# Kernel tuning notes

Measured on AMD Instinct MI355X. Metric: run time of the kernel, lower is better.

Reference implementation:

```python
import jax, jax.numpy as jnp
import numpy as np
import math

B, N, D = 64, 128, 128          # graphs, nodes per graph, d_model
D_STATE = 2                     # Mamba default d_state
D_CONV = 4                      # Mamba default conv kernel
DT_RANK = math.ceil(D / 16)     # 8
CUTOFF = 10.0
N_GAUSS = 50                    # GaussianSmearing(0, 10, 50)
EPS_RMS = 1e-5


def setup_inputs() -> dict:
    key = jax.random.key(0)
    ks = jax.random.split(key, 12)
    s = 0.05
    inp = {}
    inp['x'] = jax.random.normal(ks[0], (B * N, D), jnp.float32)
    inp['pos'] = jax.random.normal(ks[1], (B * N, 3), jnp.float32) * 5.0
    inp['map_idx'] = jax.random.randint(ks[2], (B * N,), 0, 16)
    inp['batch'] = jnp.repeat(jnp.arange(B), N)
    # RMSNorm
    inp['norm_w'] = jnp.ones((D,), jnp.float32)
    # simple message-passing gnn (stand-in for injected gnn module)
    inp['gnn_w1'] = jax.random.normal(ks[3], (D, D), jnp.float32) * s
    inp['gnn_b1'] = jnp.zeros((D,), jnp.float32)
    inp['gnn_w2'] = jax.random.normal(ks[4], (D, D), jnp.float32) * s
    inp['gnn_b2'] = jnp.zeros((D,), jnp.float32)
    # Linear(50, 1) on Gaussian-smeared edge distances
    inp['lin_w'] = jax.random.normal(ks[5], (N_GAUSS, 1), jnp.float32) * s
    inp['lin_b'] = jnp.zeros((1,), jnp.float32)
    # MambaBlock params (stored [in, out])
    inp['in_proj_w'] = jax.random.normal(ks[6], (D, 2 * D), jnp.float32) * s
    inp['conv_w'] = jax.random.normal(ks[7], (D, D_CONV), jnp.float32) * s
    inp['conv_b'] = jnp.zeros((D,), jnp.float32)
    inp['x_proj_w'] = jax.random.normal(ks[8], (D, DT_RANK + 2 * D_STATE), jnp.float32) * s
    inp['dt_proj_w'] = jax.random.normal(ks[9], (DT_RANK, D), jnp.float32) * s
    inp['dt_proj_b'] = jnp.zeros((D,), jnp.float32)
    inp['A_log'] = jnp.log(jnp.tile(jnp.arange(1, D_STATE + 1, dtype=jnp.float32), (D, 1)))
    inp['D_param'] = jnp.ones((D,), jnp.float32)
    inp['out_proj_w'] = jax.random.normal(ks[10], (D, D), jnp.float32) * s
    return inp


def _rmsnorm(x, w):
    return x * jax.lax.rsqrt(jnp.mean(x * x, axis=-1, keepdims=True) + EPS_RMS) * w


def _mamba(x_t, adj, in_proj_w, conv_w, conv_b, x_proj_w, dt_proj_w, dt_proj_b,
           A_log, D_param, out_proj_w):
    # x_t: [N, D] node sequence for one graph; adj: [N, N] dense edge-value matrix
    L = x_t.shape[0]
    A = -jnp.exp(A_log)                                   # [D, S]
    xr = x_t @ in_proj_w                                  # [L, 2D]
    xm, res = xr[:, :D], xr[:, D:]
    # causal depthwise conv1d (padding d_conv-1, truncated to L)
    xp = jnp.pad(xm, ((D_CONV - 1, 0), (0, 0)))
    xc = conv_b + sum(xp[j:j + L] * conv_w[:, j] for j in range(D_CONV))
    xc = jax.nn.silu(xc)                                  # [L, D]
    dbl = xc @ x_proj_w                                   # [L, dt_rank + 2S]
    delta = dbl[:, :DT_RANK]
    Bm = dbl[:, DT_RANK:DT_RANK + D_STATE]                # [L, S]
    Cm = dbl[:, DT_RANK + D_STATE:]                       # [L, S]
    delta = jax.nn.softplus(delta @ dt_proj_w + dt_proj_b)  # [L, D]
    # temp_adj_padded: ones [D, D] with adjacency slice in top-left
    m = min(L, D)
    adj_pad = jnp.ones((D, D), dtype=adj.dtype).at[:m, :m].set(adj[:m, :m])
    delta_p = delta @ adj_pad                             # [L, D]
    dA = jnp.exp(delta_p[:, :, None] * A[None])           # [L, D, S]
    dBu = delta_p[:, :, None] * Bm[:, None, :] * xc[:, :, None]

    def step(h, t):
        dA_t, dBu_t, C_t = t
        h = dA_t * h + dBu_t                              # [D, S]
        return h, h @ C_t                                 # [D]

    _, ys = jax.lax.scan(step, jnp.zeros((D, D_STATE), x_t.dtype), (dA, dBu, Cm))
    y = ys + xc * D_param
    y = y * jax.nn.silu(res)
    out = y @ out_proj_w
    return jnp.where(jnp.isfinite(out), out, 0.0)


def reference(x, pos, map_idx, batch, norm_w, gnn_w1, gnn_b1, gnn_w2, gnn_b2,
              lin_w, lin_b, in_proj_w, conv_w, conv_b, x_proj_w, dt_proj_w,
              dt_proj_b, A_log, D_param, out_proj_w):
    x1 = _rmsnorm(x, norm_w)                              # [B*N, D]
    xg = x1.reshape(B, N, D)
    pg = pos.reshape(B, N, 3)
    # per-graph radius graph (dense): dist + edge mask
    diff = pg[:, :, None, :] - pg[:, None, :, :]          # [B, N, N, 3]
    d2 = jnp.sum(diff * diff, axis=-1)
    eye = jnp.eye(N, dtype=bool)[None]
    dist = jnp.sqrt(jnp.where(eye, 1.0, d2))              # safe sqrt on diag
    edge_mask = (~eye) & (dist < CUTOFF)                  # [B, N, N]
    em = edge_mask.astype(x1.dtype)
    # simple message-passing gnn: mean-aggregate relu(Wx) over radius neighbors
    h = jax.nn.relu(xg @ gnn_w1 + gnn_b1)
    deg = jnp.clip(jnp.sum(em, axis=-1, keepdims=True), 1.0, None)
    agg = jnp.einsum('bij,bjd->bid', em, h) / deg
    x2 = agg @ gnn_w2 + gnn_b2                            # [B, N, D]
    # GaussianSmearing(0, 10, 50) + Linear(50, 1) -> dense edge-value matrix
    offsets = jnp.linspace(0.0, 10.0, N_GAUSS)
    coeff = -0.5 / (offsets[1] - offsets[0]) ** 2
    smear = jnp.exp(coeff * (dist[..., None] - offsets) ** 2)  # [B, N, N, 50]
    d_dense = smear @ lin_w[:, 0] + lin_b[0]
    adj = jnp.where(edge_mask, d_dense, 0.0)              # sparse-to-dense
    # Mamba mixer over each graph's node sequence
    mix = jax.vmap(lambda xt, a: _mamba(xt, a, in_proj_w, conv_w, conv_b,
                                        x_proj_w, dt_proj_w, dt_proj_b,
                                        A_log, D_param, out_proj_w))
    x3 = mix(x2, adj).reshape(B * N, D)
    output = x3 + x1
    return (output, pos, map_idx)
```

## Files before the change

### kernel.cpp

```cpp
#include <hip/hip_runtime.h>
#include <math.h>

#define B_ 64
#define N_ 128
#define D_ 128
#define BN_ 8192
#define NG_ 50
#define CUTOFF_ 10.0f

typedef __attribute__((ext_vector_type(8))) short short8v;
typedef __attribute__((ext_vector_type(4))) float f32x4;
#define MFMA16 __builtin_amdgcn_mfma_f32_16x16x32_bf16

__device__ __forceinline__ float bf2f(unsigned short h) {
    return __builtin_bit_cast(float, ((unsigned int)h) << 16);
}
__device__ __forceinline__ unsigned short f2bf(float f) {
    unsigned int u = __builtin_bit_cast(unsigned int, f);
    return (unsigned short)((u + 0x7FFFu + ((u >> 16) & 1u)) >> 16);
}
__device__ __forceinline__ void splitbf(float x, unsigned short& h, unsigned short& l) {
    h = f2bf(x);
    l = f2bf(x - bf2f(h));
}
__device__ __forceinline__ void gl_lds(const void* g, void* l) {
    __builtin_amdgcn_global_load_lds(
        (const __attribute__((address_space(1))) void*)g,
        (__attribute__((address_space(3))) void*)l, 16, 0, 0);
}

__global__ __launch_bounds__(256) void setup_k(
        const float* __restrict__ x, const float* __restrict__ norm_w,
        const float* __restrict__ pos, const int* __restrict__ mi,
        const float* __restrict__ lin_w, const float* __restrict__ lin_b,
        const float* __restrict__ w1, const float* __restrict__ w2,
        const float* __restrict__ b2, const float* __restrict__ in_proj,
        const float* __restrict__ xpw, const float* __restrict__ dtw,
        const float* __restrict__ out_proj,
        unsigned short* __restrict__ w1Th, unsigned short* __restrict__ w1Tl,
        unsigned short* __restrict__ WdTh, unsigned short* __restrict__ WdTl,
        unsigned short* __restrict__ opTh, unsigned short* __restrict__ opTl,
        unsigned short* __restrict__ WfTh, unsigned short* __restrict__ WfTl,
        float* __restrict__ bfv,
        float* __restrict__ x1f, unsigned short* __restrict__ x1h,
        unsigned short* __restrict__ x1l,
        unsigned short* __restrict__ adjh, unsigned short* __restrict__ adjl,
        unsigned short* __restrict__ emh, float* __restrict__ rdeg,
        float* __restrict__ out) {
    int blk = blockIdx.x, t = threadIdx.x;
    if (blk < 513) {
        if (blk < 128) {
            if (t < 128) {
                unsigned short h, l;
                splitbf(w1[blk * 128 + t], h, l);
                w1Th[t * 128 + blk] = h; w1Tl[t * 128 + blk] = l;
            }
        } else if (blk < 256) {
            int m = blk - 128;
            if (t < 128) {
                float s = 0.0f;
                #pragma unroll
                for (int r = 0; r < 8; r++) s = fmaf(xpw[m * 12 + r], dtw[r * 128 + t], s);
                unsigned short h, l; splitbf(s, h, l);
                WdTh[t * 128 + m] = h; WdTl[t * 128 + m] = l;
            }
        } else if (blk < 384) {
            int k = blk - 256;
            if (t < 128) {
                unsigned short h, l;
                splitbf(out_proj[k * 128 + t], h, l);
                opTh[t * 128 + k] = h; opTl[t * 128 + k] = l;
            }
        } else if (blk < 512) {
            int k = blk - 384;
            float s = 0.0f;
            #pragma unroll 8
            for (int j = 0; j < 128; j++) s = fmaf(w2[k * 128 + j], in_proj[j * 256 + t], s);
            unsigned short h, l; splitbf(s, h, l);
            WfTh[t * 128 + k] = h; WfTl[t * 128 + k] = l;
        } else {
            float s = 0.0f;
            #pragma unroll 8
            for (int j = 0; j < 128; j++) s = fmaf(b2[j], in_proj[j * 256 + t], s);
            bfv[t] = s;
        }
    } else if (blk < 642) {
        int idx = (blk - 513) * 256 + t;
        if (idx < BN_ * 3) out[(size_t)BN_ * D_ + idx] = pos[idx];
        if (idx < BN_) out[(size_t)BN_ * D_ + BN_ * 3 + idx] = (float)mi[idx];
    } else if (blk < 2690) {
        int rblk = blk - 642;
        int wv = t >> 6, ln = t & 63;
        int row = rblk * 4 + wv;
        const float2* xr = reinterpret_cast<const float2*>(x) + (size_t)row * 64;
        float2 v = xr[ln];
        float s = fmaf(v.x, v.x, v.y * v.y);
        #pragma unroll
        for (int o = 32; o > 0; o >>= 1) s += __shfl_down(s, o, 64);
        float tot = __shfl(s, 0, 64);
        float r = rsqrtf(tot * (1.0f / D_) + 1e-5f);
        float2 wv2 = reinterpret_cast<const float2*>(norm_w)[ln];
        float o0 = v.x * r * wv2.x, o1 = v.y * r * wv2.y;
        reinterpret_cast<float2*>(x1f)[(size_t)row * 64 + ln] = make_float2(o0, o1);
        unsigned short h0, l0, h1, l1;
        splitbf(o0, h0, l0); splitbf(o1, h1, l1);
        reinterpret_cast<ushort2*>(x1h)[(size_t)row * 64 + ln] = make_ushort2(h0, h1);
        reinterpret_cast<ushort2*>(x1l)[(size_t)row * 64 + ln] = make_ushort2(l0, l1);
    } else {
        __shared__ float px[N_], py[N_], pz[N_];
        __shared__ float lw[NG_];
        __shared__ int degs[8];
        int ablk = blk - 2690;
        int bx = ablk & 15, b = ablk >> 4;
        if (t < N_) {
            const float* p = pos + (size_t)(b * N_ + t) * 3;
            px[t] = p[0]; py[t] = p[1]; pz[t] = p[2];
        } else if (t - N_ < NG_) {
            lw[t - N_] = lin_w[t - N_];
        }
        if (t >= 248) degs[t - 248] = 0;
        __syncthreads();
        float linb = lin_b[0];
        int j = t & 127;
        int il = t >> 7;
        const float DEL = 10.0f / 49.0f;
        const float COEFF = -0.5f / (DEL * DEL);
        #pragma unroll
        for (int p = 0; p < 4; p++) {
            int i = bx * 8 + p * 2 + il;
            float dx = px[i] - px[j], dy = py[i] - py[j], dz = pz[i] - pz[j];
            float d2 = dx * dx + dy * dy + dz * dz;
            float dist = (i == j) ? 1.0f : sqrtf(d2);
            bool edge = (i != j) && (dist < CUTOFF_);
            float val = 0.0f;
            if (edge) {
                int g0 = (int)ceilf((dist - 1.75f) / DEL); if (g0 < 0) g0 = 0;
                int g1 = (int)floorf((dist + 1.75f) / DEL); if (g1 > NG_ - 1) g1 = NG_ - 1;
                float dm = dist - (float)g0 * DEL;
                float tg = expf(COEFF * dm * dm);
                float ug = expf(COEFF * DEL * (DEL - 2.0f * dm));
                float s = linb;
                for (int g = g0; g <= g1; g++) {
                    s = fmaf(lw[g], tg, s);
                    tg *= ug;
                    ug *= 0.36787944117144233f;
                }
                val = s;
            }
            size_t idx = ((size_t)b * N_ + i) * N_ + j;
            unsigned short h, l; splitbf(val, h, l);
            adjh[idx] = h; adjl[idx] = l;
            emh[idx] = edge ? 0x3F80 : 0;
            unsigned long long msk = __ballot(edge);
            if ((t & 63) == 0) atomicAdd(&degs[p * 2 + il], __popcll(msk));
        }
        __syncthreads();
        if (t < 8) {
            int dg = degs[t];
            rdeg[(size_t)b * N_ + bx * 8 + t] = 1.0f / (float)(dg > 0 ? dg : 1);
        }
    }
}

#define AHOFF 0
#define ALOFF 8192
#define BHOFF 16384
#define BLOFF 32768
template <int EPI, bool ALO>
__global__ __launch_bounds__(256, 3) void mgemm_k(
        const unsigned short* __restrict__ Ah, const unsigned short* __restrict__ Al,
        const unsigned short* __restrict__ BTh, const unsigned short* __restrict__ BTl,
        const float* __restrict__ bias, const float* __restrict__ AUX,
        float* __restrict__ Cf, unsigned short* __restrict__ Ch,
        unsigned short* __restrict__ Cl, int cstride, int wbs) {
    extern __shared__ char sm[];
    int tid = threadIdx.x;
    int row_base = blockIdx.x * 32;
    int col_base = blockIdx.y * 64;

    const unsigned short* pBh = BTh;
    const unsigned short* pBl = BTl;
    if (wbs) {
        size_t bo = (size_t)(row_base >> 7) * (size_t)wbs;
        pBh += bo; pBl += bo;
    }

    #pragma unroll
    for (int i = 0; i < 2; i++) {
        int s = tid + i * 256;
        int row = s >> 4, inner = s & 15;
        int gb = (inner * 16) ^ ((row & 7) << 4);
        size_t gsrc = (size_t)(row_base + row) * 256 + gb;
        gl_lds((const char*)Ah + gsrc, sm + AHOFF + s * 16);
        if (ALO) gl_lds((const char*)Al + gsrc, sm + ALOFF + s * 16);
    }
    #pragma unroll
    for (int i = 0; i < 4; i++) {
        int s = tid + i * 256;
        int n = s >> 4, inner = s & 15;
        int gb = (inner * 16) ^ ((n & 7) << 4);
        size_t gsrc = (size_t)(col_base + n) * 256 + gb;
        gl_lds((const char*)pBh + gsrc, sm + BHOFF + s * 16);
        gl_lds((const char*)pBl + gsrc, sm + BLOFF + s * 16);
    }
    __syncthreads();

    int w = tid >> 6, l = tid & 63;
    int rlow = l & 15, kb_lane = (l >> 4) * 16;
    int nB = w * 16 + rlow;
    int nswz = (nB & 7) << 4;
    f32x4 acc[2] = {{0.f, 0.f, 0.f, 0.f}, {0.f, 0.f, 0.f, 0.f}};
    #pragma unroll
    for (int kb = 0; kb < 4; kb++) {
        int kbyte = kb * 64 + kb_lane;
        short8v bh = *(const short8v*)(sm + BHOFF + nB * 256 + (kbyte ^ nswz));
        short8v bl = *(const short8v*)(sm + BLOFF + nB * 256 + (kbyte ^ nswz));
        #pragma unroll
        for (int rf = 0; rf < 2; rf++) {
            int ra = rf * 16 + rlow;
            int aswz = (ra & 7) << 4;
            short8v ah = *(const short8v*)(sm + AHOFF + ra * 256 + (kbyte ^ aswz));
            acc[rf] = MFMA16(ah, bh, acc[rf], 0, 0, 0);
            acc[rf] = MFMA16(ah, bl, acc[rf], 0, 0, 0);
            if (ALO) {
                short8v al_ = *(const short8v*)(sm + ALOFF + ra * 256 + (kbyte ^ aswz));
                acc[rf] = MFMA16(al_, bh, acc[rf], 0, 0, 0);
            }
        }
    }

    int colg = col_base + w * 16 + rlow;
    #pragma unroll
    for (int rf = 0; rf < 2; rf++) {
        int row0 = row_base + rf * 16 + (l >> 4) * 4;
        if (EPI == 1) {
            float b_ = bias[colg];
            unsigned short hh[4], ll[4];
            #pragma unroll
            for (int q = 0; q < 4; q++) {
                float t = fmaxf(acc[rf][q] + b_, 0.0f);
                splitbf(t, hh[q], ll[q]);
            }
            size_t bb = (size_t)(row0 >> 7) * 16384 + (size_t)colg * 128 + (row0 & 127);
            *reinterpret_cast<ushort4*>(Ch + bb) = make_ushort4(hh[0], hh[1], hh[2], hh[3]);
            *reinterpret_cast<ushort4*>(Cl + bb) = make_ushort4(ll[0], ll[1], ll[2], ll[3]);
        } else {
            #pragma unroll
            for (int q = 0; q < 4; q++) {
                int row = row0 + q;
                float t = acc[rf][q];
                if (EPI == 2) {
                    t *= AUX[row];
                    unsigned short h, lo; splitbf(t, h, lo);
                    Ch[(size_t)row * 128 + colg] = h;
                    Cl[(size_t)row * 128 + colg] = lo;
                }
                if (EPI == 5) {
                    t = isfinite(t) ? t : 0.0f;
                    t += AUX[(size_t)row * 128 + colg];
                    Cf[(size_t)row * cstride + colg] = t;
                }
            }
        }
    }
}

__device__ __forceinline__ void st128(char* dst, const char* g, int tid) {
    #pragma unroll
    for (int i = 0; i < 4; i++) {
        int s = tid + i * 512;
        int row = s >> 4, inner = s & 15;
        gl_lds(g + row * 256 + ((inner * 16) ^ ((row & 7) << 4)), dst + s * 16);
    }
}
__device__ __forceinline__ void stA48(char* dst, const char* g, int r0, int tid) {
    #pragma unroll
    for (int i = 0; i < 2; i++) {
        int s = tid + i * 512;
        if (s < 768) {
            int lr = s >> 4, inner = s & 15;
            int srow = r0 - 16 + lr; if (srow < 0) srow = 0;
            gl_lds(g + srow * 256 + ((inner * 16) ^ ((lr & 7) << 4)), dst + s * 16);
        }
    }
}
template <int NRF>
__device__ __forceinline__ void fpass(const char* sm, int ah, int al, int bh, int bl,
                                      int w, int l, f32x4 (&acc)[NRF]) {
    int rlow = l & 15, khi = (l >> 4) * 16;
    int nB = w * 16 + rlow;
    int nkey = (nB & 7) << 4;
    #pragma unroll
    for (int kb = 0; kb < 4; kb++) {
        int kbyte = kb * 64 + khi;
        short8v bhv = *(const short8v*)(sm + bh + nB * 256 + (kbyte ^ nkey));
        short8v blv = *(const short8v*)(sm + bl + nB * 256 + (kbyte ^ nkey));
        #pragma unroll
        for (int rf = 0; rf < NRF; rf++) {
            int ra = rf * 16 + rlow;
            int ao = ra * 256 + (kbyte ^ ((ra & 7) << 4));
            short8v ahv = *(const short8v*)(sm + ah + ao);
            short8v alv = *(const short8v*)(sm + al + ao);
            acc[rf] = MFMA16(ahv, bhv, acc[rf], 0, 0, 0);
            acc[rf] = MFMA16(ahv, blv, acc[rf], 0, 0, 0);
            acc[rf] = MFMA16(alv, bhv, acc[rf], 0, 0, 0);
        }
    }
}

__global__ __launch_bounds__(512, 2) void fused_k(
        const unsigned short* __restrict__ aggh, const unsigned short* __restrict__ aggl,
        const unsigned short* __restrict__ WfTh, const unsigned short* __restrict__ WfTl,
        const float* __restrict__ bfv,
        const float* __restrict__ conv_w, const float* __restrict__ conv_b,
        const float* __restrict__ xpw,
        const unsigned short* __restrict__ WdTh, const unsigned short* __restrict__ WdTl,
        const float* __restrict__ dtb,
        const unsigned short* __restrict__ adjh, const unsigned short* __restrict__ adjl,
        float* __restrict__ resT, float* __restrict__ xcT,
        float* __restrict__ bcT, float* __restrict__ dpT) {
    __shared__ __align__(16) char sm[163840];
    const int AH = 0, AL = 12288, XM = 24576, BH = 49152, BL = 81920,
              XCH = 114688, XCL = 122880, DH = 131072, DL = 139264, XCF = 147456;
    int blk = blockIdx.x, tid = threadIdx.x;
    int b = blk >> 2, r0 = (blk & 3) * 32;
    int w = tid >> 6, l = tid & 63;
    int rlow = l & 15, qrow = (l >> 4) * 4;

    stA48(sm + AH, (const char*)aggh + (size_t)b * 32768, r0, tid);
    stA48(sm + AL, (const char*)aggl + (size_t)b * 32768, r0, tid);
    st128(sm + BH, (const char*)WfTh, tid);
    st128(sm + BL, (const char*)WfTl, tid);
    __syncthreads();

    f32x4 acc[3] = {{0.f,0.f,0.f,0.f},{0.f,0.f,0.f,0.f},{0.f,0.f,0.f,0.f}};
    fpass<3>(sm, AH, AL, BH, BL, w, l, acc);
    __syncthreads();
    st128(sm + BH, (const char*)WfTh + 32768, tid);
    st128(sm + BL, (const char*)WfTl + 32768, tid);
    {
        int colg = w * 16 + rlow;
        float bb = bfv[colg];
        #pragma unroll
        for (int rf = 0; rf < 3; rf++) {
            #pragma unroll
            for (int q = 0; q < 4; q++) {
                int lr = rf * 16 + qrow + q;
                *(float*)(sm + XM + lr * 512 + ((colg * 4) ^ ((lr & 7) << 4))) =
                    acc[rf][q] + bb;
            }
        }
    }
    __syncthreads();

    f32x4 acc2[3] = {{0.f,0.f,0.f,0.f},{0.f,0.f,0.f,0.f},{0.f,0.f,0.f,0.f}};
    fpass<3>(sm, AH, AL, BH, BL, w, l, acc2);
    {
        int colg = w * 16 + rlow;
        float bb = bfv[128 + colg];
        #pragma unroll
        for (int rf = 1; rf < 3; rf++) {
            int lr0 = rf * 16 + qrow;
            int tt = r0 + lr0 - 16;
            float v[4];
            #pragma unroll
            for (int q = 0; q < 4; q++) {
                float rs = acc2[rf][q] + bb;
                v[q] = rs / (1.0f + expf(-rs));
            }
            *reinterpret_cast<float4*>(resT + ((size_t)b * 128 + colg) * 128 + tt) =
                make_float4(v[0], v[1], v[2], v[3]);
        }
    }
    __syncthreads();

    st128(sm + BH, (const char*)WdTh, tid);
    st128(sm + BL, (const char*)WdTl, tid);
    {
        int ot = tid >> 4, dg = tid & 15;
        float pc0 = 0, pc1 = 0, pc2 = 0, pc3 = 0;
        #pragma unroll
        for (int k = 0; k < 8; k++) {
            int d = dg * 8 + k;
            float accv = conv_b[d];
            #pragma unroll
            for (int jj = 0; jj < 4; jj++) {
                int tt = r0 + ot + jj - 3;
                if (tt >= 0) {
                    int lr = ot + jj - 3 + 16;
                    float xv = *(const float*)(sm + XM + lr * 512 +
                                               ((d * 4) ^ ((lr & 7) << 4)));
                    accv = fmaf(xv, conv_w[d * 4 + jj], accv);
                }
            }
            float xc = accv / (1.0f + expf(-accv));
            unsigned short hh, ll; splitbf(xc, hh, ll);
            int pb = ot * 256 + ((d * 2) ^ ((ot & 7) << 4));
            *(unsigned short*)(sm + XCH + pb) = hh;
            *(unsigned short*)(sm + XCL + pb) = ll;
            *(float*)(sm + XCF + ot * 512 + ((d * 4) ^ ((ot & 7) << 4))) = xc;
            float4 xw = *(const float4*)(xpw + d * 12 + 8);
            pc0 = fmaf(xc, xw.x, pc0); pc1 = fmaf(xc, xw.y, pc1);
            pc2 = fmaf(xc, xw.z, pc2); pc3 = fmaf(xc, xw.w, pc3);
        }
        #pragma unroll
        for (int m = 1; m < 16; m <<= 1) {
            pc0 += __shfl_xor(pc0, m, 64);
            pc1 += __shfl_xor(pc1, m, 64);
            pc2 += __shfl_xor(pc2, m, 64);
            pc3 += __shfl_xor(pc3, m, 64);
        }
        if (dg < 4) {
            float pv = dg == 0 ? pc0 : dg == 1 ? pc1 : dg == 2 ? pc2 : pc3;
            bcT[(size_t)b * 512 + dg * 128 + r0 + ot] = pv;
        }
    }
    __syncthreads();

    {
        int d = tid & 127, tg = tid >> 7;
        float v[8];
        #pragma unroll
        for (int k = 0; k < 8; k++) {
            int ot = tg * 8 + k;
            v[k] = *(const float*)(sm + XCF + ot * 512 + ((d * 4) ^ ((ot & 7) << 4)));
        }
        float* dst = xcT + ((size_t)b * 128 + d) * 128 + r0 + tg * 8;
        *reinterpret_cast<float4*>(dst) = make_float4(v[0], v[1], v[2], v[3]);
        *reinterpret_cast<float4*>(dst + 4) = make_float4(v[4], v[5], v[6], v[7]);
    }

    f32x4 dacc[2] = {{0.f,0.f,0.f,0.f},{0.f,0.f,0.f,0.f}};
    fpass<2>(sm, XCH, XCL, BH, BL, w, l, dacc);
    {
        int colg = w * 16 + rlow;
        float db = dtb[colg];
        #pragma unroll
        for (int rf = 0; rf < 2; rf++) {
            #pragma unroll
            for (int q = 0; q < 4; q++) {
                int lr = rf * 16 + qrow + q;
                float t = dacc[rf][q] + db;
                t = fmaxf(t, 0.0f) + log1pf(expf(-fabsf(t)));
                unsigned short hh, ll; splitbf(t, hh, ll);
                int pb = lr * 256 + ((colg * 2) ^ ((lr & 7) << 4));
                *(unsigned short*)(sm + DH + pb) = hh;
                *(unsigned short*)(sm + DL + pb) = ll;
            }
        }
    }
    __syncthreads();

    st128(sm + BH, (const char*)adjh + (size_t)b * 32768, tid);
    st128(sm + BL, (const char*)adjl + (size_t)b * 32768, tid);
    __syncthreads();
    f32x4 pacc[2] = {{0.f,0.f,0.f,0.f},{0.f,0.f,0.f,0.f}};
    fpass<2>(sm, DH, DL, BH, BL, w, l, pacc);
    {
        int colg = w * 16 + rlow;
        #pragma unroll
        for (int rf = 0; rf < 2; rf++) {
            int lr0 = rf * 16 + qrow;
            *reinterpret_cast<float4*>(dpT + ((size_t)b * 128 + colg) * 128 + r0 + lr0) =
                make_float4(pacc[rf][0], pacc[rf][1], pacc[rf][2], pacc[rf][3]);
        }
    }
}

__global__ __launch_bounds__(256) void scanout_k(
        const float* __restrict__ dpT, const float* __restrict__ xcT,
        const float* __restrict__ bcT, const float* __restrict__ resT,
        const float* __restrict__ A_log, const float* __restrict__ Dpar,
        const unsigned short* __restrict__ opTh, const unsigned short* __restrict__ opTl,
        const float* __restrict__ x1f, float* __restrict__ out) {
    __shared__ __align__(16) char smb[116736];
    float* lds = (float*)smb;
    float* bcl = (float*)(smb + 49152);
    const int YH = 51200, YL = 83968;
    int b = blockIdx.x;
    int t = threadIdx.x;
    if (t < 128) {
        float4 v = reinterpret_cast<const float4*>(bcT + (size_t)b * 512)[t];
        *reinterpret_cast<float4*>(bcl + t * 4) = v;
    }
    float a1 = 0.f, a2 = 0.f, Dp = 0.f;
    if (t < 128) {
        a1 = -expf(A_log[t * 2]);
        a2 = -expf(A_log[t * 2 + 1]);
        Dp = Dpar[t];
    }
    float h1 = 0.0f, h2 = 0.0f;
    const float4* dp4 = reinterpret_cast<const float4*>(dpT + (size_t)b * 16384);
    const float4* xc4 = reinterpret_cast<const float4*>(xcT + (size_t)b * 16384);
    const float4* rr4 = reinterpret_cast<const float4*>(resT + (size_t)b * 16384);
    for (int c = 0; c < 4; c++) {
        __syncthreads();
        #pragma unroll
        for (int k = 0; k < 4; k++) {
            int q = t + k * 256;
            int dd = q >> 3, tq = q & 7;
            int gidx = dd * 32 + c * 8 + tq;
            float4 vd = dp4[gidx], vx = xc4[gidx], vr = rr4[gidx];
            #pragma unroll
            for (int j = 0; j < 4; j++) {
                int tp = tq * 4 + j;
                int sw = dd ^ tp;
                float fd = (j == 0) ? vd.x : (j == 1) ? vd.y : (j == 2) ? vd.z : vd.w;
                float fx = (j == 0) ? vx.x : (j == 1) ? vx.y : (j == 2) ? vx.z : vx.w;
                float fr = (j == 0) ? vr.x : (j == 1) ? vr.y : (j == 2) ? vr.z : vr.w;
                lds[tp * 128 + sw] = fd;
                lds[4096 + tp * 128 + sw] = fx;
                lds[8192 + tp * 128 + sw] = fr;
            }
        }
        __syncthreads();
        if (t < 128) {
            #pragma unroll 8
            for (int tp = 0; tp < 32; tp++) {
                int sw = t ^ tp;
                float dpv = lds[tp * 128 + sw];
                float xcv = lds[4096 + tp * 128 + sw];
                float rv  = lds[8192 + tp * 128 + sw];
                int tg = c * 32 + tp;
                float bm0 = bcl[tg], bm1 = bcl[128 + tg];
                float cm0 = bcl[256 + tg], cm1 = bcl[384 + tg];
                float e1 = expf(dpv * a1), e2 = expf(dpv * a2);
                float bu = dpv * xcv;
                h1 = fmaf(e1, h1, bu * bm0);
                h2 = fmaf(e2, h2, bu * bm1);
                float y = fmaf(h1, cm0, h2 * cm1);
                float yv = fmaf(xcv, Dp, y) * rv;
                unsigned short hh, ll; splitbf(yv, hh, ll);
                int byo = (t * 2) ^ ((tg & 7) << 4);
                *(unsigned short*)(smb + YH + tg * 256 + byo) = hh;
                *(unsigned short*)(smb + YL + tg * 256 + byo) = ll;
            }
        }
    }
    __syncthreads();

    int w = t >> 6, l = t & 63;
    int rlow = l & 15, kb_lane = (l >> 4) * 16;
    int nB = w * 16 + rlow;
    int nswz = (nB & 7) << 4;
    for (int cu = 0; cu < 2; cu++) {
        #pragma unroll
        for (int i = 0; i < 4; i++) {
            int s = t + i * 256;
            int row = s >> 4, inner = s & 15;
            int gb = (inner * 16) ^ ((row & 7) << 4);
            size_t gsrc = (size_t)(cu * 64 + row) * 256 + gb;
            gl_lds((const char*)opTh + gsrc, smb + s * 16);
            gl_lds((const char*)opTl + gsrc, smb + 16384 + s * 16);
        }
        __syncthreads();
        int colg = cu * 64 + nB;
        for (int ru = 0; ru < 4; ru++) {
            f32x4 acc[2] = {{0.f, 0.f, 0.f, 0.f}, {0.f, 0.f, 0.f, 0.f}};
            #pragma unroll
            for (int kb = 0; kb < 4; kb++) {
                int kbyte = kb * 64 + kb_lane;
                short8v bh = *(const short8v*)(smb + nB * 256 + (kbyte ^ nswz));
                short8v bl = *(const short8v*)(smb + 16384 + nB * 256 + (kbyte ^ nswz));
                #pragma unroll
                for (int rf = 0; rf < 2; rf++) {
                    int ra = ru * 32 + rf * 16 + rlow;
                    int aswz = (ra & 7) << 4;
                    short8v ah = *(const short8v*)(smb + YH + ra * 256 + (kbyte ^ aswz));
                    acc[rf] = MFMA16(ah, bh, acc[rf], 0, 0, 0);
                    acc[rf] = MFMA16(ah, bl, acc[rf], 0, 0, 0);
                    short8v al_ = *(const short8v*)(smb + YL + ra * 256 + (kbyte ^ aswz));
                    acc[rf] = MFMA16(al_, bh, acc[rf], 0, 0, 0);
                }
            }
            #pragma unroll
            for (int rf = 0; rf < 2; rf++) {
                int row0 = ru * 32 + rf * 16 + (l >> 4) * 4;
                #pragma unroll
                for (int q = 0; q < 4; q++) {
                    int row = row0 + q;
                    float tv = acc[rf][q];
                    tv = isfinite(tv) ? tv : 0.0f;
                    size_t g = (size_t)(b * 128 + row) * 128 + colg;
                    out[g] = tv + x1f[g];
                }
            }
        }
        __syncthreads();
    }
}

extern "C" void kernel_launch(void* const* d_in, const int* in_sizes, int n_in,
                              void* d_out, int out_size, void* d_ws, size_t ws_size,
                              hipStream_t stream) {
    const float* x        = (const float*)d_in[0];
    const float* pos      = (const float*)d_in[1];
    const int*   mi       = (const int*)d_in[2];
    const float* norm_w   = (const float*)d_in[4];
    const float* w1       = (const float*)d_in[5];
    const float* b1       = (const float*)d_in[6];
    const float* w2       = (const float*)d_in[7];
    const float* b2       = (const float*)d_in[8];
    const float* lin_w    = (const float*)d_in[9];
    const float* lin_b    = (const float*)d_in[10];
    const float* in_proj  = (const float*)d_in[11];
    const float* conv_w   = (const float*)d_in[12];
    const float* conv_b   = (const float*)d_in[13];
    const float* xpw      = (const float*)d_in[14];
    const float* dtw      = (const float*)d_in[15];
    const float* dtb      = (const float*)d_in[16];
    const float* A_log    = (const float*)d_in[17];
    const float* Dpar     = (const float*)d_in[18];
    const float* out_proj = (const float*)d_in[19];

    float* out = (float*)d_out;
    char* base = (char*)d_ws;
    const size_t MB = 1u << 20;
    const size_t PL = 1048576;

    float* x1f  = (float*)(base);
    float* resT = (float*)(base + 8 * MB);
    float* dpT  = (float*)(base + 12 * MB);
    float* xcT  = (float*)(base + 16 * MB);
    float* bcT  = (float*)(base + 20 * MB);
    float* rdeg = (float*)(base + 20 * MB + 131072);

    unsigned short* P = (unsigned short*)(base + 21 * MB);
    unsigned short* x1h  = P +  0 * PL;
    unsigned short* x1l  = P +  1 * PL;
    unsigned short* hTh  = P +  2 * PL;
    unsigned short* hTl  = P +  3 * PL;
    unsigned short* aggh = P +  4 * PL;
    unsigned short* aggl = P +  5 * PL;
    unsigned short* xch  = P +  6 * PL;
    unsigned short* xcl  = P +  7 * PL;
    unsigned short* dlh  = P +  8 * PL;
    unsigned short* dll  = P +  9 * PL;
    unsigned short* adjh = P + 12 * PL;
    unsigned short* adjl = P + 13 * PL;
    unsigned short* emh  = P + 14 * PL;

    unsigned short* W = (unsigned short*)(base + 52 * MB);
    unsigned short* w1Th = W;
    unsigned short* w1Tl = W + 16384;
    unsigned short* WdTh = W + 2 * 16384;
    unsigned short* WdTl = W + 3 * 16384;
    unsigned short* opTh = W + 4 * 16384;
    unsigned short* opTl = W + 5 * 16384;
    unsigned short* WfTh = W + 6 * 16384;
    unsigned short* WfTl = WfTh + 32768;
    float* bfv = (float*)(WfTl + 32768);

    const size_t gsm = 49152;

    setup_k<<<3714, 256, 0, stream>>>(x, norm_w, pos, mi, lin_w, lin_b,
                                      w1, w2, b2, in_proj, xpw, dtw, out_proj,
                                      w1Th, w1Tl, WdTh, WdTl, opTh, opTl, WfTh, WfTl,
                                      bfv, x1f, x1h, x1l, adjh, adjl, emh, rdeg, out);
    mgemm_k<1, true><<<dim3(256, 2), 256, gsm, stream>>>(
        x1h, x1l, w1Th, w1Tl, b1, nullptr, nullptr, hTh, hTl, 128, 0);
    mgemm_k<2, false><<<dim3(256, 2), 256, gsm, stream>>>(
        emh, emh, hTh, hTl, nullptr, rdeg, nullptr, aggh, aggl, 128, 16384);
    fused_k<<<256, 512, 0, stream>>>(aggh, aggl, WfTh, WfTl, bfv,
                                     conv_w, conv_b, xpw, WdTh, WdTl, dtb,
                                     adjh, adjl, resT, xcT, bcT, dpT);
    scanout_k<<<B_, 256, 0, stream>>>(dpT, xcT, bcT, resT, A_log, Dpar,
                                      opTh, opTl, x1f, out);
}
```

Baseline: 83.64 us.

## Fuse GNN h-projection and neighbor aggregation GEMMs into one per-graph kernel

Replaces the two mgemm_k launches (x1@W1+relu producing hT, then em@h scaled by 1/deg) with a single hagg_k kernel that runs one 512-thread block per graph. The relu(h) tile is kept in LDS in transposed bf16 hi/lo form and consumed directly by the aggregation MFMA. This removes one launch and the global round trip of the hT intermediate. In exchange only 64 blocks run, each using 128KB of LDS, so GPU occupancy drops sharply compared with the earlier 512-block grids.

```diff
diff --git a/kernel.cpp b/kernel.cpp
--- a/kernel.cpp
+++ b/kernel.cpp
@@ -162,109 +162,6 @@
     }
 }
 
-#define AHOFF 0
-#define ALOFF 8192
-#define BHOFF 16384
-#define BLOFF 32768
-template <int EPI, bool ALO>
-__global__ __launch_bounds__(256, 3) void mgemm_k(
-        const unsigned short* __restrict__ Ah, const unsigned short* __restrict__ Al,
-        const unsigned short* __restrict__ BTh, const unsigned short* __restrict__ BTl,
-        const float* __restrict__ bias, const float* __restrict__ AUX,
-        float* __restrict__ Cf, unsigned short* __restrict__ Ch,
-        unsigned short* __restrict__ Cl, int cstride, int wbs) {
-    extern __shared__ char sm[];
-    int tid = threadIdx.x;
-    int row_base = blockIdx.x * 32;
-    int col_base = blockIdx.y * 64;
-
-    const unsigned short* pBh = BTh;
-    const unsigned short* pBl = BTl;
-    if (wbs) {
-        size_t bo = (size_t)(row_base >> 7) * (size_t)wbs;
-        pBh += bo; pBl += bo;
-    }
-
-    #pragma unroll
-    for (int i = 0; i < 2; i++) {
-        int s = tid + i * 256;
-        int row = s >> 4, inner = s & 15;
-        int gb = (inner * 16) ^ ((row & 7) << 4);
-        size_t gsrc = (size_t)(row_base + row) * 256 + gb;
-        gl_lds((const char*)Ah + gsrc, sm + AHOFF + s * 16);
-        if (ALO) gl_lds((const char*)Al + gsrc, sm + ALOFF + s * 16);
-    }
-    #pragma unroll
-    for (int i = 0; i < 4; i++) {
-        int s = tid + i * 256;
-        int n = s >> 4, inner = s & 15;
-        int gb = (inner * 16) ^ ((n & 7) << 4);
-        size_t gsrc = (size_t)(col_base + n) * 256 + gb;
-        gl_lds((const char*)pBh + gsrc, sm + BHOFF + s * 16);
-        gl_lds((const char*)pBl + gsrc, sm + BLOFF + s * 16);
-    }
-    __syncthreads();
-
-    int w = tid >> 6, l = tid & 63;
-    int rlow = l & 15, kb_lane = (l >> 4) * 16;
-    int nB = w * 16 + rlow;
-    int nswz = (nB & 7) << 4;
-    f32x4 acc[2] = {{0.f, 0.f, 0.f, 0.f}, {0.f, 0.f, 0.f, 0.f}};
-    #pragma unroll
-    for (int kb = 0; kb < 4; kb++) {
-        int kbyte = kb * 64 + kb_lane;
-        short8v bh = *(const short8v*)(sm + BHOFF + nB * 256 + (kbyte ^ nswz));
-        short8v bl = *(const short8v*)(sm + BLOFF + nB * 256 + (kbyte ^ nswz));
-        #pragma unroll
-        for (int rf = 0; rf < 2; rf++) {
-            int ra = rf * 16 + rlow;
-            int aswz = (ra & 7) << 4;
-            short8v ah = *(const short8v*)(sm + AHOFF + ra * 256 + (kbyte ^ aswz));
-            acc[rf] = MFMA16(ah, bh, acc[rf], 0, 0, 0);
-            acc[rf] = MFMA16(ah, bl, acc[rf], 0, 0, 0);
-            if (ALO) {
-                short8v al_ = *(const short8v*)(sm + ALOFF + ra * 256 + (kbyte ^ aswz));
-                acc[rf] = MFMA16(al_, bh, acc[rf], 0, 0, 0);
-            }
-        }
-    }
-
-    int colg = col_base + w * 16 + rlow;
-    #pragma unroll
-    for (int rf = 0; rf < 2; rf++) {
-        int row0 = row_base + rf * 16 + (l >> 4) * 4;
-        if (EPI == 1) {
-            float b_ = bias[colg];
-            unsigned short hh[4], ll[4];
-            #pragma unroll
-            for (int q = 0; q < 4; q++) {
-                float t = fmaxf(acc[rf][q] + b_, 0.0f);
-                splitbf(t, hh[q], ll[q]);
-            }
-            size_t bb = (size_t)(row0 >> 7) * 16384 + (size_t)colg * 128 + (row0 & 127);
-            *reinterpret_cast<ushort4*>(Ch + bb) = make_ushort4(hh[0], hh[1], hh[2], hh[3]);
-            *reinterpret_cast<ushort4*>(Cl + bb) = make_ushort4(ll[0], ll[1], ll[2], ll[3]);
-        } else {
-            #pragma unroll
-            for (int q = 0; q < 4; q++) {
-                int row = row0 + q;
-                float t = acc[rf][q];
-                if (EPI == 2) {
-                    t *= AUX[row];
-                    unsigned short h, lo; splitbf(t, h, lo);
-                    Ch[(size_t)row * 128 + colg] = h;
-                    Cl[(size_t)row * 128 + colg] = lo;
-                }
-                if (EPI == 5) {
-                    t = isfinite(t) ? t : 0.0f;
-                    t += AUX[(size_t)row * 128 + colg];
-                    Cf[(size_t)row * cstride + colg] = t;
-                }
-            }
-        }
-    }
-}
-
 __device__ __forceinline__ void st128(char* dst, const char* g, int tid) {
     #pragma unroll
     for (int i = 0; i < 4; i++) {
@@ -304,6 +201,86 @@
             acc[rf] = MFMA16(ahv, bhv, acc[rf], 0, 0, 0);
             acc[rf] = MFMA16(ahv, blv, acc[rf], 0, 0, 0);
             acc[rf] = MFMA16(alv, bhv, acc[rf], 0, 0, 0);
+        }
+    }
+}
+
+__global__ __launch_bounds__(512) void hagg_k(
+        const unsigned short* __restrict__ x1h, const unsigned short* __restrict__ x1l,
+        const unsigned short* __restrict__ w1Th, const unsigned short* __restrict__ w1Tl,
+        const float* __restrict__ b1,
+        const unsigned short* __restrict__ emh, const float* __restrict__ rdeg,
+        unsigned short* __restrict__ aggh, unsigned short* __restrict__ aggl) {
+    __shared__ __align__(16) char smb[131072];
+    const int AH = 0, AL = 32768, BH = 65536, BL = 98304;
+    int b = blockIdx.x, tid = threadIdx.x;
+    int w = tid >> 6, l = tid & 63;
+    int rlow = l & 15, khi = (l >> 4) * 16, qrow = (l >> 4) * 4;
+    int colg = w * 16 + rlow;
+    int ckey = (colg & 7) << 4;
+
+    st128(smb + AH, (const char*)x1h + (size_t)b * 32768, tid);
+    st128(smb + AL, (const char*)x1l + (size_t)b * 32768, tid);
+    st128(smb + BH, (const char*)w1Th, tid);
+    st128(smb + BL, (const char*)w1Tl, tid);
+    __syncthreads();
+
+    f32x4 acc[8];
+    #pragma unroll
+    for (int i = 0; i < 8; i++) acc[i] = (f32x4){0.f, 0.f, 0.f, 0.f};
+    fpass<8>(smb, AH, AL, BH, BL, w, l, acc);
+    __syncthreads();
+
+    {
+        float bb = b1[colg];
+        #pragma unroll
+        for (int rf = 0; rf < 8; rf++) {
+            int row0 = rf * 16 + qrow;
+            unsigned short hh[4], ll[4];
+            #pragma unroll
+            for (int q = 0; q < 4; q++) {
+                float t = fmaxf(acc[rf][q] + bb, 0.0f);
+                splitbf(t, hh[q], ll[q]);
+            }
+            int byo = (row0 * 2) ^ ckey;
+            *(ushort4*)(smb + AH + colg * 256 + byo) = make_ushort4(hh[0], hh[1], hh[2], hh[3]);
+            *(ushort4*)(smb + AL + colg * 256 + byo) = make_ushort4(ll[0], ll[1], ll[2], ll[3]);
+        }
+    }
+    st128(smb + BH, (const char*)emh + (size_t)b * 32768, tid);
+    __syncthreads();
+
+    f32x4 ag[8];
+    #pragma unroll
+    for (int i = 0; i < 8; i++) ag[i] = (f32x4){0.f, 0.f, 0.f, 0.f};
+    {
+        int nB = colg;
+        int nkey = ckey;
+        #pragma unroll
+        for (int kb = 0; kb < 4; kb++) {
+            int kbyte = kb * 64 + khi;
+            short8v bh_ = *(const short8v*)(smb + AH + nB * 256 + (kbyte ^ nkey));
+            short8v bl_ = *(const short8v*)(smb + AL + nB * 256 + (kbyte ^ nkey));
+            #pragma unroll
+            for (int rf = 0; rf < 8; rf++) {
+                int ra = rf * 16 + rlow;
+                short8v ae = *(const short8v*)(smb + BH + ra * 256 + (kbyte ^ ((ra & 7) << 4)));
+                ag[rf] = MFMA16(ae, bh_, ag[rf], 0, 0, 0);
+                ag[rf] = MFMA16(ae, bl_, ag[rf], 0, 0, 0);
+            }
+        }
+    }
+    #pragma unroll
+    for (int rf = 0; rf < 8; rf++) {
+        int row0 = rf * 16 + qrow;
+        #pragma unroll
+        for (int q = 0; q < 4; q++) {
+            int row = row0 + q;
+            float t = ag[rf][q] * rdeg[b * 128 + row];
+            unsigned short h, lo; splitbf(t, h, lo);
+            size_t g = (size_t)b * 16384 + (size_t)row * 128 + colg;
+            aggh[g] = h;
+            aggl[g] = lo;
         }
     }
 }
@@ -628,14 +605,8 @@
     unsigned short* P = (unsigned short*)(base + 21 * MB);
     unsigned short* x1h  = P +  0 * PL;
     unsigned short* x1l  = P +  1 * PL;
-    unsigned short* hTh  = P +  2 * PL;
-    unsigned short* hTl  = P +  3 * PL;
     unsigned short* aggh = P +  4 * PL;
     unsigned short* aggl = P +  5 * PL;
-    unsigned short* xch  = P +  6 * PL;
-    unsigned short* xcl  = P +  7 * PL;
-    unsigned short* dlh  = P +  8 * PL;
-    unsigned short* dll  = P +  9 * PL;
     unsigned short* adjh = P + 12 * PL;
     unsigned short* adjl = P + 13 * PL;
     unsigned short* emh  = P + 14 * PL;
@@ -651,16 +622,11 @@
     unsigned short* WfTl = WfTh + 32768;
     float* bfv = (float*)(WfTl + 32768);
 
-    const size_t gsm = 49152;
-
     setup_k<<<3714, 256, 0, stream>>>(x, norm_w, pos, mi, lin_w, lin_b,
                                       w1, w2, b2, in_proj, xpw, dtw, out_proj,
                                       w1Th, w1Tl, WdTh, WdTl, opTh, opTl, WfTh, WfTl,
                                       bfv, x1f, x1h, x1l, adjh, adjl, emh, rdeg, out);
-    mgemm_k<1, true><<<dim3(256, 2), 256, gsm, stream>>>(
-        x1h, x1l, w1Th, w1Tl, b1, nullptr, nullptr, hTh, hTl, 128, 0);
-    mgemm_k<2, false><<<dim3(256, 2), 256, gsm, stream>>>(
-        emh, emh, hTh, hTl, nullptr, rdeg, nullptr, aggh, aggl, 128, 16384);
+    hagg_k<<<B_, 512, 0, stream>>>(x1h, x1l, w1Th, w1Tl, b1, emh, rdeg, aggh, aggl);
     fused_k<<<256, 512, 0, stream>>>(aggh, aggl, WfTh, WfTl, bfv,
                                      conv_w, conv_b, xpw, WdTh, WdTl, dtb,
                                      adjh, adjl, resT, xcT, bcT, dpT);
```

Result: no change. 84.42 us (+0.9%).
